# Kernel optimization log

Measured on AMD Instinct MI355X. Metric: run time of the kernel, lower is better.

## Reference

```python
import jax, jax.numpy as jnp
import numpy as np

B, S, D, R = 8, 2048, 2048, 256


def soft_threshold24(w):
    """2:4 soft-threshold: in each contiguous group of 4 along the last dim,
    keep the top-2 |w| and shrink them by the 3rd-largest |w| (soft threshold),
    zeroing the bottom two. Mirrors soft_threshold24_triton."""
    rows, K = w.shape
    g = w.reshape(rows, K // 4, 4)
    a = jnp.abs(g)
    t = jnp.sort(a, axis=-1)[..., 1:2]  # 2nd smallest == 3rd largest per group
    sp = jnp.sign(g) * jnp.maximum(a - t, 0.0)
    return sp.reshape(rows, K)


def fp16_mm(a, b):
    """fake_fp8_mm: cast operands to fp16, matmul with fp32 accumulation/output."""
    return jnp.matmul(a.astype(jnp.float16), b.astype(jnp.float16),
                      preferred_element_type=jnp.float32)


def sparse_linear(x, w, b, scale):
    """SparseOverlayFunction.forward: 2:4-sparsified, scaled weight + fp16 GEMM."""
    x2 = x.reshape(-1, x.shape[-1])                # [N, K]
    ws = soft_threshold24(w) * scale               # [K, M], 2:4 sparse * learnable scale
    out = fp16_mm(x2, ws)                          # [N, M] fp32
    out = out.reshape(x.shape[:-1] + (w.shape[-1],))
    return out + b


def setup_inputs():
    key = jax.random.key(0)
    ks = jax.random.split(key, 4)
    x = jax.random.normal(ks[0], (B, S, D), jnp.float32)
    weight_in = jax.random.normal(ks[1], (D, R), jnp.float32) * 0.02
    weight_out = jax.random.normal(ks[2], (R, D), jnp.float32) * 0.02
    bias_in = jnp.zeros((R,), jnp.float32)
    bias_out = jax.random.normal(ks[3], (D,), jnp.float32) * 0.01
    sparse_scale_in = jnp.ones((1,), jnp.float32)
    sparse_scale_out = jnp.ones((1,), jnp.float32)
    return {"x": x, "weight_in": weight_in, "weight_out": weight_out,
            "bias_in": bias_in, "bias_out": bias_out,
            "sparse_scale_in": sparse_scale_in, "sparse_scale_out": sparse_scale_out}


def reference(x, weight_in, weight_out, bias_in, bias_out, sparse_scale_in, sparse_scale_out):
    h = sparse_linear(x, weight_in, bias_in, sparse_scale_in)    # [B,S,R]
    y = sparse_linear(h, weight_out, bias_out, sparse_scale_out)  # [B,S,D]
    return y
```

## Files before the change

### kernel.cpp

```cpp
#include <hip/hip_runtime.h>
#include <stdint.h>
#include <stddef.h>

typedef _Float16 f16;
typedef __attribute__((ext_vector_type(8))) _Float16 f16x8;
typedef __attribute__((ext_vector_type(4))) float f32x4;

#define GPTR(p) ((const __attribute__((address_space(1))) void*)(p))
#define LPTR(p) ((__attribute__((address_space(3))) void*)(p))

__device__ __forceinline__ void async16(const void* g, void* l) {
    __builtin_amdgcn_global_load_lds(GPTR(g), LPTR(l), 16, 0, 0);
}

__global__ __launch_bounds__(256) void sparsify_frag(
        const float* __restrict__ W, const float* __restrict__ scale,
        f16* __restrict__ Wf, int K, int M) {
    __shared__ f16 T[64][80];
    const int r0 = blockIdx.y << 6, m0 = blockIdx.x << 6;
    const float s = scale[0];
    const int t = threadIdx.x;
    const int rr = t >> 2, mb = (t & 3) << 4;
    const float* src = W + (size_t)(r0 + rr) * M + m0 + mb;
    #pragma unroll
    for (int j = 0; j < 4; j++) {
        float4 v = *(const float4*)(src + j * 4);
        float a0 = fabsf(v.x), a1 = fabsf(v.y), a2 = fabsf(v.z), a3 = fabsf(v.w);
        float lo1 = fminf(a0, a1), hi1 = fmaxf(a0, a1);
        float lo2 = fminf(a2, a3), hi2 = fmaxf(a2, a3);
        float th = fminf(fmaxf(lo1, lo2), fminf(hi1, hi2));
        int m = mb + j * 4;
        T[m + 0][rr] = (f16)(copysignf(fmaxf(a0 - th, 0.f), v.x) * s);
        T[m + 1][rr] = (f16)(copysignf(fmaxf(a1 - th, 0.f), v.y) * s);
        T[m + 2][rr] = (f16)(copysignf(fmaxf(a2 - th, 0.f), v.z) * s);
        T[m + 3][rr] = (f16)(copysignf(fmaxf(a3 - th, 0.f), v.w) * s);
    }
    __syncthreads();
    const int mm = t >> 2, rb = (t & 3) << 4;
    const int col = m0 + mm;
    const int Mb = M >> 4;
    #pragma unroll
    for (int h = 0; h < 2; h++) {
        int k = r0 + rb + h * 8;
        size_t blk = ((size_t)(k >> 5) * Mb + (col >> 4)) * 64
                   + (size_t)(((k >> 3) & 3) * 16 + (col & 15));
        *(f16x8*)(Wf + blk * 8) = *(const f16x8*)&T[mm][rb + h * 8];
    }
}

__global__ __launch_bounds__(256, 4) void gemm1_kernel(
        const float* __restrict__ A, const f16* __restrict__ Bf,
        const float* __restrict__ bias, f16* __restrict__ Hf) {
    constexpr int K = 2048, BK = 64, NT = K / BK;
    __shared__ float4 Asf[64 * 16];
    __shared__ f16x8  Bs[8 * 64];

    const int tid = threadIdx.x, lane = tid & 63, wv = tid >> 6;
    const int wm = wv & 1, wn = wv >> 1;
    const int lr = lane & 15, q = lane >> 4;

    const int id = blockIdx.x + (blockIdx.y << 2);
    const int xr = id & 7, xt = id >> 3;
    const int nb = xt & 3, p = xr + ((xt >> 2) << 3);
    const int row0 = p << 6, col0 = nb << 6;

    f32x4 acc[2][2] = {};

    const float* aSrc[4];
    #pragma unroll
    for (int j = 0; j < 4; j++) {
        int i = wv * 4 + j;
        int r = i * 4 + (lane >> 4);
        int c = lane & 15;
        int cs = (c & 8) | ((c & 7) ^ (r & 7));
        aSrc[j] = A + (size_t)(row0 + r) * K + cs * 4;
    }
    const f16* bSrc[2];
    #pragma unroll
    for (int j = 0; j < 2; j++) {
        int ch = wv * 2 + j;
        int s = ch >> 2, c = ch & 3;
        bSrc[j] = Bf + (((size_t)s * 16 + (col0 >> 4) + c) * 64) * 8 + lane * 8;
    }

    for (int t = 0; t < NT; ++t) {
        #pragma unroll
        for (int j = 0; j < 4; j++) {
            int i = wv * 4 + j;
            async16(aSrc[j], (char*)Asf + i * 1024);
            aSrc[j] += BK;
        }
        #pragma unroll
        for (int j = 0; j < 2; j++) {
            int ch = wv * 2 + j;
            async16(bSrc[j], (char*)Bs + ch * 1024);
            bSrc[j] += 2 * 16 * 64 * 8;
        }
        __syncthreads();
        #pragma unroll
        for (int ks = 0; ks < 2; ks++) {
            f16x8 af[2], bf[2];
            #pragma unroll
            for (int m = 0; m < 2; m++) {
                int r = wm * 32 + m * 16 + lr;
                float4 v0 = Asf[r * 16 + (ks * 8 + ((2 * q)     ^ (r & 7)))];
                float4 v1 = Asf[r * 16 + (ks * 8 + ((2 * q + 1) ^ (r & 7)))];
                f16x8 h;
                h[0] = (f16)v0.x; h[1] = (f16)v0.y; h[2] = (f16)v0.z; h[3] = (f16)v0.w;
                h[4] = (f16)v1.x; h[5] = (f16)v1.y; h[6] = (f16)v1.z; h[7] = (f16)v1.w;
                af[m] = h;
            }
            #pragma unroll
            for (int n = 0; n < 2; n++)
                bf[n] = Bs[(ks * 4 + wn * 2 + n) * 64 + lane];
            #pragma unroll
            for (int m = 0; m < 2; m++)
                #pragma unroll
                for (int n = 0; n < 2; n++)
                    acc[m][n] = __builtin_amdgcn_mfma_f32_16x16x32_f16(
                        af[m], bf[n], acc[m][n], 0, 0, 0);
        }
        __syncthreads();
    }

    #pragma unroll
    for (int m = 0; m < 2; m++) {
        int r16 = (row0 + wm * 32 + m * 16) >> 4;
        #pragma unroll
        for (int n = 0; n < 2; n++) {
            int gc = col0 + wn * 32 + n * 16 + lr;
            float bv = bias[gc];
            int kt = gc >> 5, qq = (gc >> 3) & 3, e = gc & 7;
            f16* hb = Hf + ((((size_t)kt * 1024 + r16) * 4 + qq) * 16) * 8 + e;
            #pragma unroll
            for (int rr = 0; rr < 4; rr++)
                hb[(q * 4 + rr) * 8] = (f16)(acc[m][n][rr] + bv);
        }
    }
}

__global__ __launch_bounds__(256, 4) void gemm2_kernel(
        const f16* __restrict__ Hf, const f16* __restrict__ Bf,
        const float* __restrict__ bias, float* __restrict__ Y) {
    constexpr int N = 2048, NT = 4;
    __shared__ f16x8 As[16 * 64];
    __shared__ f16x8 Bs[8 * 64];

    const int tid = threadIdx.x, lane = tid & 63, wv = tid >> 6;
    const int wm = wv & 1, wn = wv >> 1;
    const int lr = lane & 15, q = lane >> 4;

    const int id = blockIdx.x + (blockIdx.y << 5);
    const int xr = id & 7, xt = id >> 3;
    const int bx = xt & 31, by = xr + ((xt >> 5) << 3);
    const int row0 = by << 7, col0 = bx << 6;

    f32x4 acc[4][2] = {};

    for (int t = 0; t < NT; ++t) {
        int kt0 = 2 * t;
        #pragma unroll
        for (int j = 0; j < 4; j++) {
            int i = wv * 4 + j;
            int s = i >> 3, rb = i & 7;
            const f16* srcp = Hf + (((size_t)(kt0 + s) * 1024 + (row0 >> 4) + rb) * 64) * 8
                              + lane * 8;
            async16(srcp, (char*)As + i * 1024);
        }
        #pragma unroll
        for (int j = 0; j < 2; j++) {
            int ch = wv * 2 + j;
            int s = ch >> 2, c = ch & 3;
            const f16* srcp = Bf + (((size_t)(kt0 + s) * 128 + (col0 >> 4) + c) * 64) * 8
                              + lane * 8;
            async16(srcp, (char*)Bs + ch * 1024);
        }
        __syncthreads();
        #pragma unroll
        for (int ks = 0; ks < 2; ks++) {
            f16x8 af[4], bf[2];
            #pragma unroll
            for (int m = 0; m < 4; m++)
                af[m] = As[(ks * 8 + wm * 4 + m) * 64 + lane];
            #pragma unroll
            for (int n = 0; n < 2; n++)
                bf[n] = Bs[(ks * 4 + wn * 2 + n) * 64 + lane];
            #pragma unroll
            for (int m = 0; m < 4; m++)
                #pragma unroll
                for (int n = 0; n < 2; n++)
                    acc[m][n] = __builtin_amdgcn_mfma_f32_16x16x32_f16(
                        af[m], bf[n], acc[m][n], 0, 0, 0);
        }
        __syncthreads();
    }

    #pragma unroll
    for (int m = 0; m < 4; m++) {
        int gr0 = row0 + wm * 64 + m * 16 + q * 4;
        #pragma unroll
        for (int n = 0; n < 2; n++) {
            int gc = col0 + wn * 32 + n * 16 + lr;
            float bv = bias[gc];
            #pragma unroll
            for (int rr = 0; rr < 4; rr++)
                Y[(size_t)(gr0 + rr) * N + gc] = acc[m][n][rr] + bv;
        }
    }
}

extern "C" void kernel_launch(void* const* d_in, const int* in_sizes, int n_in,
                              void* d_out, int out_size, void* d_ws, size_t ws_size,
                              hipStream_t stream) {
    const float* x  = (const float*)d_in[0];
    const float* w1 = (const float*)d_in[1];
    const float* w2 = (const float*)d_in[2];
    const float* b1 = (const float*)d_in[3];
    const float* b2 = (const float*)d_in[4];
    const float* s1 = (const float*)d_in[5];
    const float* s2 = (const float*)d_in[6];
    float* y = (float*)d_out;

    constexpr int NROWS = 8 * 2048;
    constexpr int D = 2048, R = 256;

    char* ws = (char*)d_ws;
    f16* W1f = (f16*)ws;
    f16* W2f = (f16*)(ws + (2u << 20));
    f16* Hf  = (f16*)(ws + (4u << 20));

    hipLaunchKernelGGL(sparsify_frag, dim3(R / 64, D / 64), dim3(256),
                       0, stream, w1, s1, W1f, D, R);
    hipLaunchKernelGGL(sparsify_frag, dim3(D / 64, R / 64), dim3(256),
                       0, stream, w2, s2, W2f, R, D);

    hipLaunchKernelGGL(gemm1_kernel, dim3(4, NROWS / 64), dim3(256),
                       0, stream, x, W1f, b1, Hf);

    hipLaunchKernelGGL(gemm2_kernel, dim3(D / 64, NROWS / 128), dim3(256),
                       0, stream, Hf, W2f, b2, y);
}
```

Baseline: 290.7 us.

## Convert A to fp16 once in registers and load B fragments directly from global

gemm1 now loads fp32 A through registers, converts it to fp16 once per element, and stores it into a smaller fp16 LDS tile in MFMA fragment order. Previously the fp32 tile was copied asynchronously and converted redundantly by each wave reading it. B fragments are read straight from global memory into registers, bypassing LDS. This cuts LDS footprint and conversion work, but gives up the asynchronous global-to-LDS overlap, so load latency is exposed before each barrier.

```diff
diff --git a/kernel.cpp b/kernel.cpp
--- a/kernel.cpp
+++ b/kernel.cpp
@@ -52,8 +52,7 @@
         const float* __restrict__ A, const f16* __restrict__ Bf,
         const float* __restrict__ bias, f16* __restrict__ Hf) {
     constexpr int K = 2048, BK = 64, NT = K / BK;
-    __shared__ float4 Asf[64 * 16];
-    __shared__ f16x8  Bs[8 * 64];
+    __shared__ f16x8 Ash[512];
 
     const int tid = threadIdx.x, lane = tid & 63, wv = tid >> 6;
     const int wm = wv & 1, wn = wv >> 1;
@@ -66,59 +65,44 @@
 
     f32x4 acc[2][2] = {};
 
-    const float* aSrc[4];
-    #pragma unroll
-    for (int j = 0; j < 4; j++) {
-        int i = wv * 4 + j;
-        int r = i * 4 + (lane >> 4);
-        int c = lane & 15;
-        int cs = (c & 8) | ((c & 7) ^ (r & 7));
-        aSrc[j] = A + (size_t)(row0 + r) * K + cs * 4;
-    }
-    const f16* bSrc[2];
-    #pragma unroll
-    for (int j = 0; j < 2; j++) {
-        int ch = wv * 2 + j;
-        int s = ch >> 2, c = ch & 3;
-        bSrc[j] = Bf + (((size_t)s * 16 + (col0 >> 4) + c) * 64) * 8 + lane * 8;
-    }
+    const int clr = tid & 15, cq = (tid >> 4) & 3, crg = (tid >> 6) & 3;
+    const float* aSrc = A + (size_t)(row0 + crg * 16 + clr) * K + cq * 8;
+    constexpr size_t BKT = (size_t)16 * 64 * 8;
+    const f16* bBase = Bf + ((size_t)(col0 >> 4) + wn * 2) * 64 * 8 + lane * 8;
 
     for (int t = 0; t < NT; ++t) {
-        #pragma unroll
-        for (int j = 0; j < 4; j++) {
-            int i = wv * 4 + j;
-            async16(aSrc[j], (char*)Asf + i * 1024);
-            aSrc[j] += BK;
-        }
-        #pragma unroll
-        for (int j = 0; j < 2; j++) {
-            int ch = wv * 2 + j;
-            async16(bSrc[j], (char*)Bs + ch * 1024);
-            bSrc[j] += 2 * 16 * 64 * 8;
-        }
-        __syncthreads();
+        const f16* bp = bBase + (size_t)(2 * t) * BKT;
+        f16x8 bf[2][2];
+        bf[0][0] = *(const f16x8*)(bp);
+        bf[0][1] = *(const f16x8*)(bp + 64 * 8);
+        bf[1][0] = *(const f16x8*)(bp + BKT);
+        bf[1][1] = *(const f16x8*)(bp + BKT + 64 * 8);
+
+        float4 v0 = *(const float4*)(aSrc);
+        float4 v1 = *(const float4*)(aSrc + 4);
+        float4 v2 = *(const float4*)(aSrc + 32);
+        float4 v3 = *(const float4*)(aSrc + 36);
+        aSrc += BK;
+        f16x8 h0, h1;
+        h0[0] = (f16)v0.x; h0[1] = (f16)v0.y; h0[2] = (f16)v0.z; h0[3] = (f16)v0.w;
+        h0[4] = (f16)v1.x; h0[5] = (f16)v1.y; h0[6] = (f16)v1.z; h0[7] = (f16)v1.w;
+        h1[0] = (f16)v2.x; h1[1] = (f16)v2.y; h1[2] = (f16)v2.z; h1[3] = (f16)v2.w;
+        h1[4] = (f16)v3.x; h1[5] = (f16)v3.y; h1[6] = (f16)v3.z; h1[7] = (f16)v3.w;
+        Ash[tid]       = h0;
+        Ash[tid + 256] = h1;
+        __syncthreads();
+
         #pragma unroll
         for (int ks = 0; ks < 2; ks++) {
-            f16x8 af[2], bf[2];
-            #pragma unroll
-            for (int m = 0; m < 2; m++) {
-                int r = wm * 32 + m * 16 + lr;
-                float4 v0 = Asf[r * 16 + (ks * 8 + ((2 * q)     ^ (r & 7)))];
-                float4 v1 = Asf[r * 16 + (ks * 8 + ((2 * q + 1) ^ (r & 7)))];
-                f16x8 h;
-                h[0] = (f16)v0.x; h[1] = (f16)v0.y; h[2] = (f16)v0.z; h[3] = (f16)v0.w;
-                h[4] = (f16)v1.x; h[5] = (f16)v1.y; h[6] = (f16)v1.z; h[7] = (f16)v1.w;
-                af[m] = h;
-            }
-            #pragma unroll
-            for (int n = 0; n < 2; n++)
-                bf[n] = Bs[(ks * 4 + wn * 2 + n) * 64 + lane];
+            f16x8 af[2];
+            af[0] = Ash[(ks * 4 + wm * 2 + 0) * 64 + lane];
+            af[1] = Ash[(ks * 4 + wm * 2 + 1) * 64 + lane];
             #pragma unroll
             for (int m = 0; m < 2; m++)
                 #pragma unroll
                 for (int n = 0; n < 2; n++)
                     acc[m][n] = __builtin_amdgcn_mfma_f32_16x16x32_f16(
-                        af[m], bf[n], acc[m][n], 0, 0, 0);
+                        af[m], bf[ks][n], acc[m][n], 0, 0, 0);
         }
         __syncthreads();
     }
```

Measured after the change: 311.5 us. 7.2% more time.
